# Optimization experiments

Hardware: AMD Instinct MI355X
Metric: run time of the kernel (lower is better)

## Reference

```python
import jax, jax.numpy as jnp
import numpy as np

D_MODEL, N_HEADS, D_HEAD, D_FF, N_LAYERS, VOCAB = 768, 12, 64, 3072, 4, 32000
B, S = 4, 1024
EPS = 1e-5
NEG = -1000000000.0


def layer_norm(x, gamma, beta):
    mean = jnp.mean(x, axis=-1, keepdims=True)
    var = jnp.mean((x - mean) ** 2, axis=-1, keepdims=True)
    return gamma * ((x - mean) / jnp.sqrt(var + EPS)) + beta


def gelu_lean(x):
    return x * (0.5 * (1.0 + jnp.tanh(0.7978845608 * (x + 0.044715 * x * x * x))))


def positional_encoding(seq_len, dim, dtype):
    idx = jnp.arange(dim)
    exponent = (2 * (idx // 2)).astype(dtype) / float(dim)
    pos = jnp.arange(seq_len, dtype=dtype)[:, None]
    angle = pos / jnp.power(jnp.asarray(10000.0, dtype), exponent[None, :])
    return jnp.where((idx % 2 == 0)[None, :], jnp.sin(angle), jnp.cos(angle))


def setup_inputs() -> dict:
    key = jax.random.key(0)
    ks = jax.random.split(key, 10)
    std = 0.02
    inp = {
        "tokens": jax.random.randint(ks[0], (B, S), 0, VOCAB),
        "predict_idx": 1023,
        "embedding": std * jax.random.normal(ks[1], (D_MODEL, VOCAB), jnp.float32),
        "ln1_g": jnp.ones((N_LAYERS, D_MODEL), jnp.float32),
        "ln1_b": jnp.zeros((N_LAYERS, D_MODEL), jnp.float32),
        "wq": std * jax.random.normal(ks[2], (N_LAYERS, N_HEADS, D_HEAD, D_MODEL), jnp.float32),
        "wk": std * jax.random.normal(ks[3], (N_LAYERS, N_HEADS, D_HEAD, D_MODEL), jnp.float32),
        "wv": std * jax.random.normal(ks[4], (N_LAYERS, N_HEADS, D_HEAD, D_MODEL), jnp.float32),
        "wo": std * jax.random.normal(ks[5], (N_LAYERS, D_MODEL, N_HEADS * D_HEAD), jnp.float32),
        "ln2_g": jnp.ones((N_LAYERS, D_MODEL), jnp.float32),
        "ln2_b": jnp.zeros((N_LAYERS, D_MODEL), jnp.float32),
        "fc1": std * jax.random.normal(ks[6], (N_LAYERS, D_FF, D_MODEL), jnp.float32),
        "fc2": std * jax.random.normal(ks[7], (N_LAYERS, D_MODEL, D_FF), jnp.float32),
        "lnf_g": jnp.ones((D_MODEL,), jnp.float32),
        "lnf_b": jnp.zeros((D_MODEL,), jnp.float32),
        "unembed": std * jax.random.normal(ks[8], (VOCAB, D_MODEL), jnp.float32),
    }
    return inp


def reference(tokens, predict_idx, embedding, ln1_g, ln1_b, wq, wk, wv, wo,
              ln2_g, ln2_b, fc1, fc2, lnf_g, lnf_b, unembed):
    dtype = embedding.dtype
    b, s = tokens.shape
    d_head = wq.shape[2]
    scale = 1.0 / float(np.sqrt(d_head))

    # token embedding [B,S,D] + sinusoidal positions
    x = embedding.T[tokens] + positional_encoding(s, embedding.shape[0], dtype)[None]

    # causal mask: True above the diagonal -> filled with -1e9
    causal = jnp.triu(jnp.ones((s, s), bool), k=1)

    for l in range(wq.shape[0]):
        h = layer_norm(x, ln1_g[l], ln1_b[l])
        q = jnp.einsum('bsd,hed->bhse', h, wq[l])
        k = jnp.einsum('bsd,hed->bhse', h, wk[l])
        v = jnp.einsum('bsd,hed->bhse', h, wv[l])
        scores = jnp.einsum('bhse,bhte->bhst', q, k) * scale
        scores = jnp.where(causal[None, None], NEG, scores)
        weights = jax.nn.softmax(scores, axis=-1)
        attn = jnp.einsum('bhst,bhte->bhse', weights, v)  # [B,H,S,dh]
        attn = attn.transpose(0, 2, 1, 3).reshape(b, s, -1)  # concat heads
        x = x + attn @ wo[l].T
        h2 = layer_norm(x, ln2_g[l], ln2_b[l])
        x = x + gelu_lean(h2 @ fc1[l].T) @ fc2[l].T

    selected = x[:, predict_idx, :]  # [B, D]
    normed = layer_norm(selected, lnf_g, lnf_b)
    return normed @ unembed.T  # [B, vocab]
```

## Files before the change

kernel.cpp:

```cpp
#include <hip/hip_runtime.h>
#include <hip/hip_bf16.h>

#define D_MODEL 768
#define N_HEADS 12
#define D_HEAD  64
#define D_FF    3072
#define N_LAYERS 4
#define VOCAB   32000
#define BATCH   4
#define SEQ     1024
#define NROWS   (BATCH*SEQ)
#define NEGV    -1000000000.0f
#define LN_EPS  1e-5f

typedef __attribute__((ext_vector_type(8))) short bf16x8;
typedef __attribute__((ext_vector_type(4))) float f32x4;
typedef __attribute__((ext_vector_type(8))) unsigned short u16x8;

typedef __attribute__((address_space(1))) const unsigned int g_u32;
typedef __attribute__((address_space(3))) unsigned int l_u32;

__device__ __forceinline__ float bf2f(unsigned short u) {
  return __uint_as_float(((unsigned int)u) << 16);
}
__device__ __forceinline__ unsigned short f2bf(float f) {
  __hip_bfloat16 h = __float2bfloat16(f);
  return *reinterpret_cast<unsigned short*>(&h);
}

__device__ __forceinline__ float block_reduce_sum(float v, float* sbuf) {
#pragma unroll
  for (int off = 32; off > 0; off >>= 1) v += __shfl_down(v, off, 64);
  int lane = threadIdx.x & 63, wid = threadIdx.x >> 6;
  if (lane == 0) sbuf[wid] = v;
  __syncthreads();
  if (threadIdx.x == 0) sbuf[4] = sbuf[0] + sbuf[1] + sbuf[2] + sbuf[3];
  __syncthreads();
  return sbuf[4];
}

__device__ __forceinline__ float gelu_f(float x) {
  float c = x + 0.044715f * x * x * x;
  return x * (0.5f * (1.0f + tanhf(0.7978845608f * c)));
}

__global__ __launch_bounds__(256) void convert_kernel(
    const float* __restrict__ src, __hip_bfloat16* __restrict__ dst, int n)
{
  int i = (blockIdx.x * 256 + threadIdx.x) * 8;
  if (i >= n) return;
  float4 a = *(const float4*)(src + i);
  float4 b = *(const float4*)(src + i + 4);
  struct bf8 { __hip_bfloat16 h[8]; } r;
  r.h[0] = __float2bfloat16(a.x); r.h[1] = __float2bfloat16(a.y);
  r.h[2] = __float2bfloat16(a.z); r.h[3] = __float2bfloat16(a.w);
  r.h[4] = __float2bfloat16(b.x); r.h[5] = __float2bfloat16(b.y);
  r.h[6] = __float2bfloat16(b.z); r.h[7] = __float2bfloat16(b.w);
  *(bf8*)(dst + i) = r;
}

__global__ __launch_bounds__(256) void qkv_pack_kernel(
    const float* __restrict__ wq, const float* __restrict__ wk,
    const float* __restrict__ wv, __hip_bfloat16* __restrict__ dst)
{
  const int WMAT = D_MODEL * D_MODEL;
  long long i = (long long)(blockIdx.x * 256 + threadIdx.x) * 8;
  long long l = i / (3LL * WMAT);
  long long rem = i - l * 3LL * WMAT;
  int which = (int)(rem / WMAT);
  long long off = rem - (long long)which * WMAT;
  const float* src = (which == 0 ? wq : which == 1 ? wk : wv) + l * WMAT + off;
  float4 a = *(const float4*)src;
  float4 b = *(const float4*)(src + 4);
  struct bf8 { __hip_bfloat16 h[8]; } r;
  r.h[0] = __float2bfloat16(a.x); r.h[1] = __float2bfloat16(a.y);
  r.h[2] = __float2bfloat16(a.z); r.h[3] = __float2bfloat16(a.w);
  r.h[4] = __float2bfloat16(b.x); r.h[5] = __float2bfloat16(b.y);
  r.h[6] = __float2bfloat16(b.z); r.h[7] = __float2bfloat16(b.w);
  *(bf8*)(dst + i) = r;
}

__global__ __launch_bounds__(256) void transpose_emb_kernel(
    const float* __restrict__ emb, __hip_bfloat16* __restrict__ embT)
{
  __shared__ float tile[64][65];
  const int vb = blockIdx.x * 64;
  const int db = blockIdx.y * 64;
  const int tid = threadIdx.x;
  {
    int r = tid >> 4, c = (tid & 15) * 4;
#pragma unroll
    for (int p = 0; p < 4; ++p) {
      float4 v = *(const float4*)(emb + (size_t)(db + r + p * 16) * VOCAB + vb + c);
      tile[c + 0][r + p * 16] = v.x;
      tile[c + 1][r + p * 16] = v.y;
      tile[c + 2][r + p * 16] = v.z;
      tile[c + 3][r + p * 16] = v.w;
    }
  }
  __syncthreads();
  {
    int v = tid >> 2, d0 = (tid & 3) * 16;
    unsigned short* op = (unsigned short*)embT + (size_t)(vb + v) * D_MODEL + db + d0;
    u16x8 o0, o1;
#pragma unroll
    for (int j = 0; j < 8; ++j) {
      o0[j] = f2bf(tile[v][d0 + j]);
      o1[j] = f2bf(tile[v][d0 + 8 + j]);
    }
    *(u16x8*)op = o0;
    *(u16x8*)(op + 8) = o1;
  }
}

__global__ __launch_bounds__(256) void embed_kernel(
    const int* __restrict__ tokens, const __hip_bfloat16* __restrict__ embT,
    float* __restrict__ x)
{
  int bs = blockIdx.x;
  int s = bs & (SEQ - 1);
  int tok = tokens[bs];
  const unsigned short* ep = (const unsigned short*)embT + (size_t)tok * D_MODEL;
  for (int d = threadIdx.x; d < D_MODEL; d += 256) {
    float ev = bf2f(ep[d]);
    int dpair = d & ~1;
    float expo = (float)dpair * (1.0f / (float)D_MODEL);
    float ang = (float)s / powf(10000.0f, expo);
    float pe = (d & 1) ? cosf(ang) : sinf(ang);
    x[(size_t)bs * D_MODEL + d] = ev + pe;
  }
}

__global__ __launch_bounds__(256) void ln_kernel(
    const float* __restrict__ in, __hip_bfloat16* __restrict__ out,
    const float* __restrict__ g, const float* __restrict__ bb)
{
  __shared__ float sbuf[8];
  size_t row = blockIdx.x;
  const float* rp = in + row * D_MODEL;
  int t = threadIdx.x;
  float x0 = rp[t], x1 = rp[t + 256], x2 = rp[t + 512];
  float mean = block_reduce_sum(x0 + x1 + x2, sbuf) * (1.0f / (float)D_MODEL);
  float d0 = x0 - mean, d1 = x1 - mean, d2 = x2 - mean;
  float var = block_reduce_sum(d0*d0 + d1*d1 + d2*d2, sbuf) * (1.0f / (float)D_MODEL);
  float rstd = rsqrtf(var + LN_EPS);
  __hip_bfloat16* op = out + row * D_MODEL;
  op[t]       = __float2bfloat16(g[t]       * (d0 * rstd) + bb[t]);
  op[t + 256] = __float2bfloat16(g[t + 256] * (d1 * rstd) + bb[t + 256]);
  op[t + 512] = __float2bfloat16(g[t + 512] * (d2 * rstd) + bb[t + 512]);
}

__global__ __launch_bounds__(256) void final_ln_kernel(
    const float* __restrict__ x, const int* __restrict__ pidx,
    const float* __restrict__ g, const float* __restrict__ bb,
    float* __restrict__ out)
{
  __shared__ float sbuf[8];
  int p = pidx[0];
  const float* rp = x + ((size_t)blockIdx.x * SEQ + p) * D_MODEL;
  int t = threadIdx.x;
  float x0 = rp[t], x1 = rp[t + 256], x2 = rp[t + 512];
  float mean = block_reduce_sum(x0 + x1 + x2, sbuf) * (1.0f / (float)D_MODEL);
  float d0 = x0 - mean, d1 = x1 - mean, d2 = x2 - mean;
  float var = block_reduce_sum(d0*d0 + d1*d1 + d2*d2, sbuf) * (1.0f / (float)D_MODEL);
  float rstd = rsqrtf(var + LN_EPS);
  float* op = out + (size_t)blockIdx.x * D_MODEL;
  op[t]       = g[t]       * (d0 * rstd) + bb[t];
  op[t + 256] = g[t + 256] * (d1 * rstd) + bb[t + 256];
  op[t + 512] = g[t + 512] * (d2 * rstd) + bb[t + 512];
}

__device__ __forceinline__ int2 xcd_tile(int gx, int gy) {
  int flat = blockIdx.y * gx + blockIdx.x;
  int cpx = (gx * gy) >> 3;
  int logical = (flat & 7) * cpx + (flat >> 3);
  return make_int2(logical % gx, logical / gx);
}

__global__ __launch_bounds__(256) void gemm_bf16_kernel(
    const __hip_bfloat16* __restrict__ A, const __hip_bfloat16* __restrict__ W,
    void* __restrict__ Cv, const float* __restrict__ resid,
    int N, int K, int mode)
{
  __shared__ __align__(16) unsigned short As[2][128 * 64];
  __shared__ __align__(16) unsigned short Bs[2][128 * 64];
  const unsigned short* Au = (const unsigned short*)A;
  const unsigned short* Wu = (const unsigned short*)W;
  const int tid = threadIdx.x;
  const int wv = tid >> 6, ln = tid & 63;
  const int l15 = ln & 15, l4 = ln >> 4;
  int2 tc = xcd_tile(N >> 7, gridDim.y);
  const int bm = tc.y * 128, bn = tc.x * 128;
  const int wr = wv >> 1, wc = wv & 1;

  const int srow = wv * 8 + (ln >> 3);
  const int scg  = (ln & 7) ^ (ln >> 3);
  const size_t gofs_a = (size_t)(bm + srow) * K + scg * 8;
  const size_t gofs_b = (size_t)(bn + srow) * K + scg * 8;
  const size_t rstride = (size_t)32 * K;

#define STAGE128(buf, k0)                                                    \
  {                                                                          \
    _Pragma("unroll")                                                        \
    for (int r = 0; r < 4; ++r) {                                            \
      const unsigned short* ga = Au + gofs_a + r * rstride + (k0);           \
      const unsigned short* gb = Wu + gofs_b + r * rstride + (k0);           \
      unsigned short* la = As[buf] + (size_t)(r * 256 + wv * 64) * 8;        \
      unsigned short* lb = Bs[buf] + (size_t)(r * 256 + wv * 64) * 8;        \
      __builtin_amdgcn_global_load_lds((g_u32*)ga, (l_u32*)la, 16, 0, 0);    \
      __builtin_amdgcn_global_load_lds((g_u32*)gb, (l_u32*)lb, 16, 0, 0);    \
    }                                                                        \
  }

  f32x4 acc[4][4];
#pragma unroll
  for (int m = 0; m < 4; ++m)
#pragma unroll
    for (int n = 0; n < 4; ++n) acc[m][n] = (f32x4){0.f, 0.f, 0.f, 0.f};

  const int NT = K >> 6;
  STAGE128(0, 0);
  int cur = 0;
  for (int t = 0; t < NT; ++t) {
    __syncthreads();
    if (t + 1 < NT) STAGE128(cur ^ 1, (t + 1) << 6);
#pragma unroll
    for (int ks = 0; ks < 2; ++ks) {
      const int cl = (ks * 4 + l4) ^ (l15 & 7);
      bf16x8 af[4], bfr[4];
#pragma unroll
      for (int m = 0; m < 4; ++m)
        af[m] = *(const bf16x8*)(As[cur] + (size_t)(wr * 64 + m * 16 + l15) * 64 + cl * 8);
#pragma unroll
      for (int n = 0; n < 4; ++n)
        bfr[n] = *(const bf16x8*)(Bs[cur] + (size_t)(wc * 64 + n * 16 + l15) * 64 + cl * 8);
#pragma unroll
      for (int m = 0; m < 4; ++m)
#pragma unroll
        for (int n = 0; n < 4; ++n)
          acc[m][n] = __builtin_amdgcn_mfma_f32_16x16x32_bf16(af[m], bfr[n], acc[m][n], 0, 0, 0);
    }
    cur ^= 1;
  }

  float* Cf = (float*)Cv;
  __hip_bfloat16* Cb = (__hip_bfloat16*)Cv;
#pragma unroll
  for (int m = 0; m < 4; ++m) {
#pragma unroll
    for (int n = 0; n < 4; ++n) {
#pragma unroll
      for (int r = 0; r < 4; ++r) {
        int row = bm + wr * 64 + m * 16 + l4 * 4 + r;
        int col = bn + wc * 64 + n * 16 + l15;
        size_t off = (size_t)row * N + col;
        float v = acc[m][n][r];
        if (mode == 0)      Cf[off] = v;
        else if (mode == 1) Cf[off] = v + resid[off];
        else if (mode == 2) Cb[off] = __float2bfloat16(v);
        else                Cb[off] = __float2bfloat16(gelu_f(v));
      }
    }
  }
}

__global__ __launch_bounds__(256) void gemm64_bf16_kernel(
    const __hip_bfloat16* __restrict__ A, const __hip_bfloat16* __restrict__ W,
    void* __restrict__ Cv, const float* __restrict__ resid,
    int N, int K, int mode)
{
  __shared__ __align__(16) unsigned short As[2][64 * 64];
  __shared__ __align__(16) unsigned short Bs[2][64 * 64];
  const unsigned short* Au = (const unsigned short*)A;
  const unsigned short* Wu = (const unsigned short*)W;
  const int tid = threadIdx.x;
  const int wv = tid >> 6, ln = tid & 63;
  const int l15 = ln & 15, l4 = ln >> 4;
  int2 tc = xcd_tile(N >> 6, gridDim.y);
  const int bm = tc.y * 64, bn = tc.x * 64;
  const int wr = wv >> 1, wc = wv & 1;

  const int srow = wv * 8 + (ln >> 3);
  const int scg  = (ln & 7) ^ (ln >> 3);
  const size_t gofs_a = (size_t)(bm + srow) * K + scg * 8;
  const size_t gofs_b = (size_t)(bn + srow) * K + scg * 8;
  const size_t rstride = (size_t)32 * K;

#define STAGE64(buf, k0)                                                     \
  {                                                                          \
    _Pragma("unroll")                                                        \
    for (int r = 0; r < 2; ++r) {                                            \
      const unsigned short* ga = Au + gofs_a + r * rstride + (k0);           \
      const unsigned short* gb = Wu + gofs_b + r * rstride + (k0);           \
      unsigned short* la = As[buf] + (size_t)(r * 256 + wv * 64) * 8;        \
      unsigned short* lb = Bs[buf] + (size_t)(r * 256 + wv * 64) * 8;        \
      __builtin_amdgcn_global_load_lds((g_u32*)ga, (l_u32*)la, 16, 0, 0);    \
      __builtin_amdgcn_global_load_lds((g_u32*)gb, (l_u32*)lb, 16, 0, 0);    \
    }                                                                        \
  }

  f32x4 acc[2][2];
#pragma unroll
  for (int m = 0; m < 2; ++m)
#pragma unroll
    for (int n = 0; n < 2; ++n) acc[m][n] = (f32x4){0.f, 0.f, 0.f, 0.f};

  const int NT = K >> 6;
  STAGE64(0, 0);
  int cur = 0;
  for (int t = 0; t < NT; ++t) {
    __syncthreads();
    if (t + 1 < NT) STAGE64(cur ^ 1, (t + 1) << 6);
#pragma unroll
    for (int ks = 0; ks < 2; ++ks) {
      const int cl = (ks * 4 + l4) ^ (l15 & 7);
      bf16x8 af[2], bfr[2];
#pragma unroll
      for (int m = 0; m < 2; ++m)
        af[m] = *(const bf16x8*)(As[cur] + (size_t)(wr * 32 + m * 16 + l15) * 64 + cl * 8);
#pragma unroll
      for (int n = 0; n < 2; ++n)
        bfr[n] = *(const bf16x8*)(Bs[cur] + (size_t)(wc * 32 + n * 16 + l15) * 64 + cl * 8);
#pragma unroll
      for (int m = 0; m < 2; ++m)
#pragma unroll
        for (int n = 0; n < 2; ++n)
          acc[m][n] = __builtin_amdgcn_mfma_f32_16x16x32_bf16(af[m], bfr[n], acc[m][n], 0, 0, 0);
    }
    cur ^= 1;
  }

  float* Cf = (float*)Cv;
  __hip_bfloat16* Cb = (__hip_bfloat16*)Cv;
#pragma unroll
  for (int m = 0; m < 2; ++m) {
#pragma unroll
    for (int n = 0; n < 2; ++n) {
#pragma unroll
      for (int r = 0; r < 4; ++r) {
        int row = bm + wr * 32 + m * 16 + l4 * 4 + r;
        int col = bn + wc * 32 + n * 16 + l15;
        size_t off = (size_t)row * N + col;
        float v = acc[m][n][r];
        if (mode == 0)      Cf[off] = v;
        else if (mode == 1) Cf[off] = v + resid[off];
        else if (mode == 2) Cb[off] = __float2bfloat16(v);
        else                Cb[off] = __float2bfloat16(gelu_f(v));
      }
    }
  }
}

__global__ __launch_bounds__(256) void flash_attn_kernel(
    const __hip_bfloat16* __restrict__ qkv_, __hip_bfloat16* __restrict__ attn_)
{
  const unsigned short* qkv = (const unsigned short*)qkv_;
  unsigned short* attn = (unsigned short*)attn_;
  const int s0 = blockIdx.x * 64;
  const int h  = blockIdx.y;
  const int b  = blockIdx.z;
  const int tid = threadIdx.x;
  const int wq = tid >> 6, ln = tid & 63;
  const int l15 = ln & 15, l4 = ln >> 4;

  __shared__ unsigned short Ks[64 * 64];
  __shared__ unsigned short Vt[64 * 64];
  __shared__ unsigned short Pw[4][16 * 64];

  bf16x8 qf[2];
  {
    const size_t qbase = (size_t)(b * SEQ + s0 + wq * 16 + l15) * 2304 + h * 64;
#pragma unroll
    for (int ks = 0; ks < 2; ++ks) {
      u16x8 raw = *(const u16x8*)(qkv + qbase + ks * 32 + l4 * 8);
      bf16x8 q;
#pragma unroll
      for (int j = 0; j < 8; ++j) q[j] = (short)f2bf(bf2f(raw[j]) * 0.125f);
      qf[ks] = q;
    }
  }

  float mrow[4], lrow[4];
  f32x4 o[4];
#pragma unroll
  for (int r = 0; r < 4; ++r) { mrow[r] = -1e30f; lrow[r] = 0.f; }
#pragma unroll
  for (int n = 0; n < 4; ++n) o[n] = (f32x4){0.f, 0.f, 0.f, 0.f};

  for (int t0 = 0; t0 <= s0; t0 += 64) {
    __syncthreads();

#pragma unroll
    for (int r = 0; r < 2; ++r) {
      int o128 = wq * 2 + r;
      int t = o128 * 8 + (ln >> 3);
      int db = (ln & 7) ^ (ln >> 3);
      const unsigned short* gk =
          qkv + (size_t)(b * SEQ + t0 + t) * 2304 + 768 + h * 64 + db * 8;
      __builtin_amdgcn_global_load_lds((g_u32*)gk, (l_u32*)(Ks + o128 * 512), 16, 0, 0);
    }

    {
      int vt = tid >> 2, ec = (tid & 3) * 16;
      const unsigned short* gv =
          qkv + (size_t)(b * SEQ + t0 + vt) * 2304 + 1536 + h * 64 + ec;
      u16x8 v0 = *(const u16x8*)gv;
      u16x8 v1 = *(const u16x8*)(gv + 8);
      int tb = vt >> 3, tr = vt & 7;
#pragma unroll
      for (int j = 0; j < 8; ++j) {
        int e0 = ec + j, e1 = ec + 8 + j;
        Vt[e0 * 64 + ((tb ^ (e0 & 7)) << 3) + tr] = (unsigned short)v0[j];
        Vt[e1 * 64 + ((tb ^ (e1 & 7)) << 3) + tr] = (unsigned short)v1[j];
      }
    }
    __syncthreads();

    f32x4 sf[4];
#pragma unroll
    for (int n = 0; n < 4; ++n) sf[n] = (f32x4){0.f, 0.f, 0.f, 0.f};
#pragma unroll
    for (int ks = 0; ks < 2; ++ks) {
#pragma unroll
      for (int n = 0; n < 4; ++n) {
        int t = n * 16 + l15;
        bf16x8 kf = *(const bf16x8*)(Ks + t * 64 + (((ks * 4 + l4) ^ (t & 7)) << 3));
        sf[n] = __builtin_amdgcn_mfma_f32_16x16x32_bf16(qf[ks], kf, sf[n], 0, 0, 0);
      }
    }

    if (t0 == s0) {
#pragma unroll
      for (int n = 0; n < 4; ++n) {
        int t = n * 16 + l15;
#pragma unroll
        for (int r = 0; r < 4; ++r) {
          int q = wq * 16 + l4 * 4 + r;
          if (t > q) sf[n][r] = NEGV;
        }
      }
    }

    float pbuf[4][4];
#pragma unroll
    for (int r = 0; r < 4; ++r) {
      float rmax = fmaxf(fmaxf(sf[0][r], sf[1][r]), fmaxf(sf[2][r], sf[3][r]));
#pragma unroll
      for (int m = 1; m < 16; m <<= 1) rmax = fmaxf(rmax, __shfl_xor(rmax, m, 64));
      float mnew = fmaxf(mrow[r], rmax);
      float alpha = __expf(mrow[r] - mnew);
      float part = 0.f;
#pragma unroll
      for (int n = 0; n < 4; ++n) {
        float p = __expf(sf[n][r] - mnew);
        pbuf[n][r] = p;
        part += p;
      }
#pragma unroll
      for (int m = 1; m < 16; m <<= 1) part += __shfl_xor(part, m, 64);
      lrow[r] = lrow[r] * alpha + part;
      mrow[r] = mnew;
#pragma unroll
      for (int n = 0; n < 4; ++n) o[n][r] *= alpha;
    }

    unsigned short* Pme = Pw[wq];
#pragma unroll
    for (int n = 0; n < 4; ++n) {
      int tb = (n * 16 + l15) >> 3, tr = l15 & 7;
#pragma unroll
      for (int r = 0; r < 4; ++r) {
        int q = l4 * 4 + r;
        Pme[q * 64 + ((tb ^ (q & 7)) << 3) + tr] = f2bf(pbuf[n][r]);
      }
    }

#pragma unroll
    for (int ks = 0; ks < 2; ++ks) {
      bf16x8 pf = *(const bf16x8*)(Pme + l15 * 64 + (((ks * 4 + l4) ^ (l15 & 7)) << 3));
#pragma unroll
      for (int n = 0; n < 4; ++n) {
        int e = n * 16 + l15;
        bf16x8 vf = *(const bf16x8*)(Vt + e * 64 + (((ks * 4 + l4) ^ (e & 7)) << 3));
        o[n] = __builtin_amdgcn_mfma_f32_16x16x32_bf16(pf, vf, o[n], 0, 0, 0);
      }
    }
  }

#pragma unroll
  for (int r = 0; r < 4; ++r) {
    float inv = 1.0f / lrow[r];
    size_t base = (size_t)(b * SEQ + s0 + wq * 16 + l4 * 4 + r) * D_MODEL + h * 64;
#pragma unroll
    for (int n = 0; n < 4; ++n)
      attn[base + n * 16 + l15] = f2bf(o[n][r] * inv);
  }
}

__global__ __launch_bounds__(256) void logits_kernel(
    const float* __restrict__ normed, const float* __restrict__ unemb,
    float* __restrict__ out)
{
  __shared__ __align__(16) float ns[BATCH][D_MODEL];
  for (int d = threadIdx.x; d < BATCH * D_MODEL; d += 256)
    ((float*)ns)[d] = normed[d];
  __syncthreads();
  int g = threadIdx.x >> 4, li = threadIdx.x & 15;
  int v = blockIdx.x * 16 + g;
  const float* up = unemb + (size_t)v * D_MODEL;
  float s0 = 0.f, s1 = 0.f, s2 = 0.f, s3 = 0.f;
#pragma unroll
  for (int it = 0; it < D_MODEL / 64; ++it) {
    int e = it * 64 + li * 4;
    float4 u = *(const float4*)(up + e);
    float4 n0 = *(const float4*)&ns[0][e];
    float4 n1 = *(const float4*)&ns[1][e];
    float4 n2 = *(const float4*)&ns[2][e];
    float4 n3 = *(const float4*)&ns[3][e];
    s0 += u.x*n0.x + u.y*n0.y + u.z*n0.z + u.w*n0.w;
    s1 += u.x*n1.x + u.y*n1.y + u.z*n1.z + u.w*n1.w;
    s2 += u.x*n2.x + u.y*n2.y + u.z*n2.z + u.w*n2.w;
    s3 += u.x*n3.x + u.y*n3.y + u.z*n3.z + u.w*n3.w;
  }
#pragma unroll
  for (int msk = 1; msk < 16; msk <<= 1) {
    s0 += __shfl_xor(s0, msk, 64); s1 += __shfl_xor(s1, msk, 64);
    s2 += __shfl_xor(s2, msk, 64); s3 += __shfl_xor(s3, msk, 64);
  }
  if (li == 0) {
    out[(size_t)0 * VOCAB + v] = s0;
    out[(size_t)1 * VOCAB + v] = s1;
    out[(size_t)2 * VOCAB + v] = s2;
    out[(size_t)3 * VOCAB + v] = s3;
  }
}

extern "C" void kernel_launch(void* const* d_in, const int* in_sizes, int n_in,
                              void* d_out, int out_size, void* d_ws, size_t ws_size,
                              hipStream_t stream) {
  const int*   tokens = (const int*)d_in[0];
  const int*   pidx   = (const int*)d_in[1];
  const float* emb    = (const float*)d_in[2];
  const float* ln1_g  = (const float*)d_in[3];
  const float* ln1_b  = (const float*)d_in[4];
  const float* wq     = (const float*)d_in[5];
  const float* wk     = (const float*)d_in[6];
  const float* wv     = (const float*)d_in[7];
  const float* wo     = (const float*)d_in[8];
  const float* ln2_g  = (const float*)d_in[9];
  const float* ln2_b  = (const float*)d_in[10];
  const float* fc1    = (const float*)d_in[11];
  const float* fc2    = (const float*)d_in[12];
  const float* lnf_g  = (const float*)d_in[13];
  const float* lnf_b  = (const float*)d_in[14];
  const float* unemb  = (const float*)d_in[15];
  float* out = (float*)d_out;

  char* wp = (char*)d_ws;
  const size_t NX = (size_t)NROWS * D_MODEL;
  float* x = (float*)wp;                  wp += NX * 4;
  float* normed = (float*)wp;             wp += BATCH * D_MODEL * 4;
  __hip_bfloat16* h    = (__hip_bfloat16*)wp; wp += NX * 2;
  __hip_bfloat16* attn = (__hip_bfloat16*)wp; wp += NX * 2;
  __hip_bfloat16* qkvb = (__hip_bfloat16*)wp; wp += (size_t)NROWS * 2304 * 2;
  __hip_bfloat16* ffn  = (__hip_bfloat16*)wp; wp += (size_t)NROWS * D_FF * 2;
  __hip_bfloat16* wqkvb = (__hip_bfloat16*)wp; wp += (size_t)N_LAYERS * 2304 * D_MODEL * 2;
  __hip_bfloat16* wob   = (__hip_bfloat16*)wp; wp += (size_t)N_LAYERS * D_MODEL * D_MODEL * 2;
  __hip_bfloat16* fc1b  = (__hip_bfloat16*)wp; wp += (size_t)N_LAYERS * D_FF * D_MODEL * 2;
  __hip_bfloat16* fc2b  = (__hip_bfloat16*)wp; wp += (size_t)N_LAYERS * D_MODEL * D_FF * 2;

  __hip_bfloat16* embT = attn;

  const int WMAT = D_MODEL * D_MODEL;
  const int FMAT = D_FF * D_MODEL;

  transpose_emb_kernel<<<dim3(VOCAB / 64, D_MODEL / 64), 256, 0, stream>>>(emb, embT);
  embed_kernel<<<NROWS, 256, 0, stream>>>(tokens, embT, x);

  qkv_pack_kernel<<<N_LAYERS * 3 * WMAT / 2048, 256, 0, stream>>>(wq, wk, wv, wqkvb);
  convert_kernel<<<N_LAYERS * WMAT / 2048, 256, 0, stream>>>(wo,  wob,  N_LAYERS * WMAT);
  convert_kernel<<<N_LAYERS * FMAT / 2048, 256, 0, stream>>>(fc1, fc1b, N_LAYERS * FMAT);
  convert_kernel<<<N_LAYERS * FMAT / 2048, 256, 0, stream>>>(fc2, fc2b, N_LAYERS * FMAT);

  for (int l = 0; l < N_LAYERS; ++l) {
    const size_t qofs = (size_t)l * 3 * WMAT;
    const size_t wofs = (size_t)l * WMAT;
    const size_t fofs = (size_t)l * FMAT;

    ln_kernel<<<NROWS, 256, 0, stream>>>(x, h, ln1_g + l * D_MODEL, ln1_b + l * D_MODEL);

    gemm_bf16_kernel<<<dim3(2304 / 128, NROWS / 128), 256, 0, stream>>>(
        h, wqkvb + qofs, qkvb, nullptr, 2304, D_MODEL, 2);

    flash_attn_kernel<<<dim3(SEQ / 64, N_HEADS, BATCH), 256, 0, stream>>>(qkvb, attn);

    gemm64_bf16_kernel<<<dim3(D_MODEL / 64, NROWS / 64), 256, 0, stream>>>(
        attn, wob + wofs, x, x, D_MODEL, D_MODEL, 1);

    ln_kernel<<<NROWS, 256, 0, stream>>>(x, h, ln2_g + l * D_MODEL, ln2_b + l * D_MODEL);

    gemm_bf16_kernel<<<dim3(D_FF / 128, NROWS / 128), 256, 0, stream>>>(
        h, fc1b + fofs, ffn, nullptr, D_FF, D_MODEL, 3);

    gemm64_bf16_kernel<<<dim3(D_MODEL / 64, NROWS / 64), 256, 0, stream>>>(
        ffn, fc2b + fofs, x, x, D_MODEL, D_FF, 1);
  }

  final_ln_kernel<<<BATCH, 256, 0, stream>>>(x, pidx, lnf_g, lnf_b, normed);
  logits_kernel<<<VOCAB / 16, 256, 0, stream>>>(normed, unemb, out);
}
```

Measured before the change: 956.8 us.

## Triple-buffer GEMM K-loop with 32-wide tiles and explicit vmcnt waits

Both bf16 GEMM kernels switch from a double-buffered 64-wide K tile to a three-stage ring of 32-wide K tiles. Loads are issued two stages ahead, and the barrier waits only on the older outstanding loads through explicit s_waitcnt vmcnt. MFMA blocks are wrapped in s_setprio, and the LDS swizzle is reworked for 32-element rows. The goal is to hide global-to-LDS latency better. In exchange there are twice as many barriers per K, and correctness now relies on hand-counted vmcnt values.

```diff
diff --git a/kernel.cpp b/kernel.cpp
--- a/kernel.cpp
+++ b/kernel.cpp
@@ -177,13 +177,18 @@
   return make_int2(logical % gx, logical / gx);
 }
 
+#define WAITV4() asm volatile("s_waitcnt vmcnt(4)" ::: "memory")
+#define WAITV2() asm volatile("s_waitcnt vmcnt(2)" ::: "memory")
+#define WAITV0() asm volatile("s_waitcnt vmcnt(0)" ::: "memory")
+#define MEMFENCE() asm volatile("" ::: "memory")
+
 __global__ __launch_bounds__(256) void gemm_bf16_kernel(
     const __hip_bfloat16* __restrict__ A, const __hip_bfloat16* __restrict__ W,
     void* __restrict__ Cv, const float* __restrict__ resid,
     int N, int K, int mode)
 {
-  __shared__ __align__(16) unsigned short As[2][128 * 64];
-  __shared__ __align__(16) unsigned short Bs[2][128 * 64];
+  __shared__ __align__(16) unsigned short As[3][128 * 32];
+  __shared__ __align__(16) unsigned short Bs[3][128 * 32];
   const unsigned short* Au = (const unsigned short*)A;
   const unsigned short* Wu = (const unsigned short*)W;
   const int tid = threadIdx.x;
@@ -193,23 +198,40 @@
   const int bm = tc.y * 128, bn = tc.x * 128;
   const int wr = wv >> 1, wc = wv & 1;
 
-  const int srow = wv * 8 + (ln >> 3);
-  const int scg  = (ln & 7) ^ (ln >> 3);
-  const size_t gofs_a = (size_t)(bm + srow) * K + scg * 8;
-  const size_t gofs_b = (size_t)(bn + srow) * K + scg * 8;
-  const size_t rstride = (size_t)32 * K;
-
-#define STAGE128(buf, k0)                                                    \
-  {                                                                          \
-    _Pragma("unroll")                                                        \
-    for (int r = 0; r < 4; ++r) {                                            \
-      const unsigned short* ga = Au + gofs_a + r * rstride + (k0);           \
-      const unsigned short* gb = Wu + gofs_b + r * rstride + (k0);           \
-      unsigned short* la = As[buf] + (size_t)(r * 256 + wv * 64) * 8;        \
-      unsigned short* lb = Bs[buf] + (size_t)(r * 256 + wv * 64) * 8;        \
-      __builtin_amdgcn_global_load_lds((g_u32*)ga, (l_u32*)la, 16, 0, 0);    \
-      __builtin_amdgcn_global_load_lds((g_u32*)gb, (l_u32*)lb, 16, 0, 0);    \
-    }                                                                        \
+  const int lrow = wv * 16 + (ln >> 2);
+  const int schunk = (ln & 3) ^ ((ln >> 3) & 3);
+  const size_t gA0 = (size_t)(bm + lrow) * K + schunk * 8;
+  const size_t gA1 = (size_t)(bm + 64 + lrow) * K + schunk * 8;
+  const size_t gB0 = (size_t)(bn + lrow) * K + schunk * 8;
+  const size_t gB1 = (size_t)(bn + 64 + lrow) * K + schunk * 8;
+  const int ldsb = wv * 512;
+
+#define STAGE128(buf, k0)                                                          \
+  {                                                                                \
+    __builtin_amdgcn_global_load_lds((g_u32*)(Au + gA0 + (k0)), (l_u32*)(As[buf] + ldsb), 16, 0, 0);        \
+    __builtin_amdgcn_global_load_lds((g_u32*)(Au + gA1 + (k0)), (l_u32*)(As[buf] + 2048 + ldsb), 16, 0, 0); \
+    __builtin_amdgcn_global_load_lds((g_u32*)(Wu + gB0 + (k0)), (l_u32*)(Bs[buf] + ldsb), 16, 0, 0);        \
+    __builtin_amdgcn_global_load_lds((g_u32*)(Wu + gB1 + (k0)), (l_u32*)(Bs[buf] + 2048 + ldsb), 16, 0, 0); \
+  }
+
+  const int rslot = (l4 ^ ((l15 >> 1) & 3)) * 8;
+
+#define COMPUTE128(buf)                                                            \
+  {                                                                                \
+    bf16x8 af[4], bfr[4];                                                          \
+    _Pragma("unroll")                                                              \
+    for (int m = 0; m < 4; ++m)                                                    \
+      af[m] = *(const bf16x8*)(As[buf] + (wr * 64 + m * 16 + l15) * 32 + rslot);   \
+    _Pragma("unroll")                                                              \
+    for (int n = 0; n < 4; ++n)                                                    \
+      bfr[n] = *(const bf16x8*)(Bs[buf] + (wc * 64 + n * 16 + l15) * 32 + rslot);  \
+    __builtin_amdgcn_s_setprio(1);                                                 \
+    _Pragma("unroll")                                                              \
+    for (int m = 0; m < 4; ++m)                                                    \
+      _Pragma("unroll")                                                            \
+      for (int n = 0; n < 4; ++n)                                                  \
+        acc[m][n] = __builtin_amdgcn_mfma_f32_16x16x32_bf16(af[m], bfr[n], acc[m][n], 0, 0, 0); \
+    __builtin_amdgcn_s_setprio(0);                                                 \
   }
 
   f32x4 acc[4][4];
@@ -218,30 +240,25 @@
 #pragma unroll
     for (int n = 0; n < 4; ++n) acc[m][n] = (f32x4){0.f, 0.f, 0.f, 0.f};
 
-  const int NT = K >> 6;
+  const int NT = K >> 5;
   STAGE128(0, 0);
+  STAGE128(1, 32);
   int cur = 0;
-  for (int t = 0; t < NT; ++t) {
-    __syncthreads();
-    if (t + 1 < NT) STAGE128(cur ^ 1, (t + 1) << 6);
-#pragma unroll
-    for (int ks = 0; ks < 2; ++ks) {
-      const int cl = (ks * 4 + l4) ^ (l15 & 7);
-      bf16x8 af[4], bfr[4];
-#pragma unroll
-      for (int m = 0; m < 4; ++m)
-        af[m] = *(const bf16x8*)(As[cur] + (size_t)(wr * 64 + m * 16 + l15) * 64 + cl * 8);
-#pragma unroll
-      for (int n = 0; n < 4; ++n)
-        bfr[n] = *(const bf16x8*)(Bs[cur] + (size_t)(wc * 64 + n * 16 + l15) * 64 + cl * 8);
-#pragma unroll
-      for (int m = 0; m < 4; ++m)
-#pragma unroll
-        for (int n = 0; n < 4; ++n)
-          acc[m][n] = __builtin_amdgcn_mfma_f32_16x16x32_bf16(af[m], bfr[n], acc[m][n], 0, 0, 0);
-    }
-    cur ^= 1;
-  }
+  for (int t = 0; t < NT - 1; ++t) {
+    WAITV4();
+    __builtin_amdgcn_s_barrier();
+    MEMFENCE();
+    if (t + 2 < NT) {
+      int nxt = cur + 2; if (nxt >= 3) nxt -= 3;
+      STAGE128(nxt, (t + 2) << 5);
+    }
+    COMPUTE128(cur);
+    cur = (cur == 2) ? 0 : cur + 1;
+  }
+  WAITV0();
+  __builtin_amdgcn_s_barrier();
+  MEMFENCE();
+  COMPUTE128(cur);
 
   float* Cf = (float*)Cv;
   __hip_bfloat16* Cb = (__hip_bfloat16*)Cv;
@@ -262,6 +279,8 @@
       }
     }
   }
+#undef STAGE128
+#undef COMPUTE128
 }
 
 __global__ __launch_bounds__(256) void gemm64_bf16_kernel(
@@ -269,8 +288,8 @@
     void* __restrict__ Cv, const float* __restrict__ resid,
     int N, int K, int mode)
 {
-  __shared__ __align__(16) unsigned short As[2][64 * 64];
-  __shared__ __align__(16) unsigned short Bs[2][64 * 64];
+  __shared__ __align__(16) unsigned short As[3][64 * 32];
+  __shared__ __align__(16) unsigned short Bs[3][64 * 32];
   const unsigned short* Au = (const unsigned short*)A;
   const unsigned short* Wu = (const unsigned short*)W;
   const int tid = threadIdx.x;
@@ -280,23 +299,36 @@
   const int bm = tc.y * 64, bn = tc.x * 64;
   const int wr = wv >> 1, wc = wv & 1;
 
-  const int srow = wv * 8 + (ln >> 3);
-  const int scg  = (ln & 7) ^ (ln >> 3);
-  const size_t gofs_a = (size_t)(bm + srow) * K + scg * 8;
-  const size_t gofs_b = (size_t)(bn + srow) * K + scg * 8;
-  const size_t rstride = (size_t)32 * K;
-
-#define STAGE64(buf, k0)                                                     \
-  {                                                                          \
-    _Pragma("unroll")                                                        \
-    for (int r = 0; r < 2; ++r) {                                            \
-      const unsigned short* ga = Au + gofs_a + r * rstride + (k0);           \
-      const unsigned short* gb = Wu + gofs_b + r * rstride + (k0);           \
-      unsigned short* la = As[buf] + (size_t)(r * 256 + wv * 64) * 8;        \
-      unsigned short* lb = Bs[buf] + (size_t)(r * 256 + wv * 64) * 8;        \
-      __builtin_amdgcn_global_load_lds((g_u32*)ga, (l_u32*)la, 16, 0, 0);    \
-      __builtin_amdgcn_global_load_lds((g_u32*)gb, (l_u32*)lb, 16, 0, 0);    \
-    }                                                                        \
+  const int lrow = wv * 16 + (ln >> 2);
+  const int schunk = (ln & 3) ^ ((ln >> 3) & 3);
+  const size_t gA0 = (size_t)(bm + lrow) * K + schunk * 8;
+  const size_t gB0 = (size_t)(bn + lrow) * K + schunk * 8;
+  const int ldsb = wv * 512;
+
+#define STAGE64(buf, k0)                                                           \
+  {                                                                                \
+    __builtin_amdgcn_global_load_lds((g_u32*)(Au + gA0 + (k0)), (l_u32*)(As[buf] + ldsb), 16, 0, 0); \
+    __builtin_amdgcn_global_load_lds((g_u32*)(Wu + gB0 + (k0)), (l_u32*)(Bs[buf] + ldsb), 16, 0, 0); \
+  }
+
+  const int rslot = (l4 ^ ((l15 >> 1) & 3)) * 8;
+
+#define COMPUTE64(buf)                                                             \
+  {                                                                                \
+    bf16x8 af[2], bfr[2];                                                          \
+    _Pragma("unroll")                                                              \
+    for (int m = 0; m < 2; ++m)                                                    \
+      af[m] = *(const bf16x8*)(As[buf] + (wr * 32 + m * 16 + l15) * 32 + rslot);   \
+    _Pragma("unroll")                                                              \
+    for (int n = 0; n < 2; ++n)                                                    \
+      bfr[n] = *(const bf16x8*)(Bs[buf] + (wc * 32 + n * 16 + l15) * 32 + rslot);  \
+    __builtin_amdgcn_s_setprio(1);                                                 \
+    _Pragma("unroll")                                                              \
+    for (int m = 0; m < 2; ++m)                                                    \
+      _Pragma("unroll")                                                            \
+      for (int n = 0; n < 2; ++n)                                                  \
+        acc[m][n] = __builtin_amdgcn_mfma_f32_16x16x32_bf16(af[m], bfr[n], acc[m][n], 0, 0, 0); \
+    __builtin_amdgcn_s_setprio(0);                                                 \
   }
 
   f32x4 acc[2][2];
@@ -305,30 +337,25 @@
 #pragma unroll
     for (int n = 0; n < 2; ++n) acc[m][n] = (f32x4){0.f, 0.f, 0.f, 0.f};
 
-  const int NT = K >> 6;
+  const int NT = K >> 5;
   STAGE64(0, 0);
+  STAGE64(1, 32);
   int cur = 0;
-  for (int t = 0; t < NT; ++t) {
-    __syncthreads();
-    if (t + 1 < NT) STAGE64(cur ^ 1, (t + 1) << 6);
-#pragma unroll
-    for (int ks = 0; ks < 2; ++ks) {
-      const int cl = (ks * 4 + l4) ^ (l15 & 7);
-      bf16x8 af[2], bfr[2];
-#pragma unroll
-      for (int m = 0; m < 2; ++m)
-        af[m] = *(const bf16x8*)(As[cur] + (size_t)(wr * 32 + m * 16 + l15) * 64 + cl * 8);
-#pragma unroll
-      for (int n = 0; n < 2; ++n)
-        bfr[n] = *(const bf16x8*)(Bs[cur] + (size_t)(wc * 32 + n * 16 + l15) * 64 + cl * 8);
-#pragma unroll
-      for (int m = 0; m < 2; ++m)
-#pragma unroll
-        for (int n = 0; n < 2; ++n)
-          acc[m][n] = __builtin_amdgcn_mfma_f32_16x16x32_bf16(af[m], bfr[n], acc[m][n], 0, 0, 0);
-    }
-    cur ^= 1;
-  }
+  for (int t = 0; t < NT - 1; ++t) {
+    WAITV2();
+    __builtin_amdgcn_s_barrier();
+    MEMFENCE();
+    if (t + 2 < NT) {
+      int nxt = cur + 2; if (nxt >= 3) nxt -= 3;
+      STAGE64(nxt, (t + 2) << 5);
+    }
+    COMPUTE64(cur);
+    cur = (cur == 2) ? 0 : cur + 1;
+  }
+  WAITV0();
+  __builtin_amdgcn_s_barrier();
+  MEMFENCE();
+  COMPUTE64(cur);
 
   float* Cf = (float*)Cv;
   __hip_bfloat16* Cb = (__hip_bfloat16*)Cv;
@@ -349,6 +376,8 @@
       }
     }
   }
+#undef STAGE64
+#undef COMPUTE64
 }
 
 __global__ __launch_bounds__(256) void flash_attn_kernel(
```

Measured after the change: 925.5 us. 1.03x faster.
